# Kernel optimization log

Hardware: AMD Instinct MI355X
Metric: run time of the kernel (lower is better)

Reference implementation:

```python
import jax, jax.numpy as jnp
import numpy as np


def setup_inputs() -> dict:
    key = jax.random.key(0)
    k1, k2, k3 = jax.random.split(key, 3)
    x = jax.random.normal(k1, (32, 256, 56, 56), dtype=jnp.float32)
    att_w = jax.random.normal(k2, (4, 256), dtype=jnp.float32) * 0.05  # 1x1 attention conv weight (K, Cin)
    weight = jax.random.normal(k3, (4, 256, 256, 3, 3), dtype=jnp.float32) * 0.05  # (K, Cout, Cin, kh, kw)
    return {"x": x, "att_w": att_w, "weight": weight}


def reference(x, att_w, weight):
    # x: (B, Cin, H, W); att_w: (K, Cin); weight: (K, Cout, Cin, kh, kw)
    # Attention: global avg pool -> 1x1 conv (Cin->K) -> sigmoid  (named softmax_att but is sigmoid)
    pooled = jnp.mean(x, axis=(2, 3))                 # (B, Cin)
    att = jax.nn.sigmoid(pooled @ att_w.T)            # (B, K)
    # Per-sample expert-mixed conv kernels
    agg_w = jnp.einsum('bk,koihw->boihw', att, weight)  # (B, Cout, Cin, kh, kw)

    def conv_one(xi, wi):
        # xi: (Cin, H, W), wi: (Cout, Cin, kh, kw)
        return jax.lax.conv_general_dilated(
            xi[None], wi,
            window_strides=(1, 1),
            padding=[(1, 1), (1, 1)],
            rhs_dilation=(1, 1),
            dimension_numbers=('NCHW', 'OIHW', 'NCHW'),
        )[0]

    out = jax.vmap(conv_one)(x, agg_w)                # (B, Cout, H, W)
    return out
```

## Files before the change

kernel.cpp:

```cpp
#include <hip/hip_runtime.h>

typedef __attribute__((ext_vector_type(8))) short short8;
typedef __attribute__((ext_vector_type(4))) float floatx4;

__device__ __forceinline__ unsigned short bf16_rne(float f) {
  unsigned int u = __builtin_bit_cast(unsigned int, f);
  u += 0x7fffu + ((u >> 16) & 1u);
  return (unsigned short)(u >> 16);
}

__device__ __forceinline__ void glds16(const void* g, void* l) {
  __builtin_amdgcn_global_load_lds((const __attribute__((address_space(1))) void*)g,
                                   (__attribute__((address_space(3))) void*)l, 16, 0, 0);
}


__global__ void zero_pk_kernel(float* __restrict__ pk) {
  pk[threadIdx.x] = 0.f;
}

__global__ __launch_bounds__(256) void prep_kernel(const float* __restrict__ x,
                                                   const float* __restrict__ att_w,
                                                   unsigned short* __restrict__ xpad,
                                                   float* __restrict__ pooledk) {
  const int bid = blockIdx.x;
  const int b   = bid / 196;
  const int rem = bid - b * 196;
  const int cig = rem / 49;
  const int spc = rem - cig * 49;
  const int t  = threadIdx.x;
  const int cs = t >> 6, sl = t & 63;
  const int sp0 = spc * 64;

  __shared__ unsigned short T2[64 * 72];
  __shared__ float red[4][4];

  const float* xrow = x + (size_t)(b * 256 + cig * 64 + cs * 16) * 3136 + sp0 + sl;
  float v[16];
  #pragma unroll
  for (int i = 0; i < 16; ++i) v[i] = xrow[(size_t)i * 3136];

  float acc0 = 0.f, acc1 = 0.f, acc2 = 0.f, acc3 = 0.f;
  #pragma unroll
  for (int i = 0; i < 16; ++i) {
    const int ci = cig * 64 + cs * 16 + i;
    acc0 += v[i] * att_w[0 * 256 + ci];
    acc1 += v[i] * att_w[1 * 256 + ci];
    acc2 += v[i] * att_w[2 * 256 + ci];
    acc3 += v[i] * att_w[3 * 256 + ci];
  }
  #pragma unroll
  for (int o = 32; o > 0; o >>= 1) {
    acc0 += __shfl_xor(acc0, o, 64);
    acc1 += __shfl_xor(acc1, o, 64);
    acc2 += __shfl_xor(acc2, o, 64);
    acc3 += __shfl_xor(acc3, o, 64);
  }
  if (sl == 0) { red[cs][0] = acc0; red[cs][1] = acc1; red[cs][2] = acc2; red[cs][3] = acc3; }

  short8 w0, w1;
  #pragma unroll
  for (int i = 0; i < 8; ++i) w0[i] = (short)bf16_rne(v[i]);
  #pragma unroll
  for (int i = 0; i < 8; ++i) w1[i] = (short)bf16_rne(v[8 + i]);
  *(short8*)(T2 + sl * 72 + cs * 16) = w0;
  *(short8*)(T2 + sl * 72 + cs * 16 + 8) = w1;
  __syncthreads();

  if (t < 4) {
    float s = red[0][t] + red[1][t] + red[2][t] + red[3][t];
    atomicAdd(&pooledk[b * 4 + t], s);
  }

  unsigned short* xb = xpad + (size_t)b * (8 * 3364 * 32);
  #pragma unroll
  for (int it = 0; it < 2; ++it) {
    const int c = it * 256 + t;
    const int spl = c >> 3, oc8 = c & 7;
    const int cg8 = cig * 8 + oc8;
    const int kc = cg8 >> 2, o2 = cg8 & 3;
    const int spg = sp0 + spl;
    const int h = spg / 56, wc = spg - h * 56;
    const int pos = (h + 1) * 58 + (wc + 1);
    const short8 vv = *(const short8*)(T2 + spl * 72 + oc8 * 8);
    *(short8*)(xb + (size_t)kc * (3364 * 32) + pos * 32 + o2 * 8) = vv;
  }
}

__global__ __launch_bounds__(256) void border_kernel(unsigned short* __restrict__ xpad) {
  const int b = blockIdx.x, quarter = blockIdx.y, t = threadIdx.x;
  const short8 z = {0, 0, 0, 0, 0, 0, 0, 0};
  unsigned short* xb = xpad + (size_t)b * (8 * 3364 * 32);
  for (int it = 0; it < 8; ++it) {
    const int idx = it * 256 + t;
    if (idx >= 1824) break;
    const int s8 = idx & 3, kc = (idx >> 2) & 7, j = idx >> 5;
    const int pi = quarter * 57 + j;
    int h2, w2;
    if (pi < 58)       { h2 = 0;  w2 = pi; }
    else if (pi < 116) { h2 = 57; w2 = pi - 58; }
    else { const int k = pi - 116; h2 = 1 + (k >> 1); w2 = (k & 1) * 57; }
    *(short8*)(xb + (size_t)kc * (3364 * 32) + (h2 * 58 + w2) * 32 + s8 * 8) = z;
  }
}

__global__ __launch_bounds__(256) void agg_kernel(const float* __restrict__ w,
                                                  const float* __restrict__ pooledk,
                                                  unsigned short* __restrict__ agg) {
  const int co = blockIdx.x;
  const int bq = blockIdx.y;
  const int t = threadIdx.x;
  __shared__ float W[4][2304];
  __shared__ float attl[16];
  if (t < 16) {
    const float z = pooledk[bq * 16 + t] * (1.f / 3136.f);
    attl[t] = 1.f / (1.f + expf(-z));
  }
  #pragma unroll
  for (int e = 0; e < 4; ++e) {
    const float* src = w + (size_t)(e * 256 + co) * 2304;
    #pragma unroll
    for (int j = 0; j < 9; ++j) W[e][j * 256 + t] = src[j * 256 + t];
  }
  __syncthreads();

  #pragma unroll
  for (int rep = 0; rep < 2; ++rep) {
    const int id = rep * 256 + t;
    if (id < 288) {
      const int kc  = id / 36;
      const int rm  = id - kc * 36;
      const int rs  = rm >> 2;
      const int oct = rm & 3;
      const int wib = (kc * 32 + oct * 8) * 9 + rs;
      const int off = (kc * 9 + rs) * 8192 + co * 32 + oct * 8;
      float w0[8], w1[8], w2[8], w3[8];
      #pragma unroll
      for (int u = 0; u < 8; ++u) {
        w0[u] = W[0][wib + u * 9];
        w1[u] = W[1][wib + u * 9];
        w2[u] = W[2][wib + u * 9];
        w3[u] = W[3][wib + u * 9];
      }
      #pragma unroll
      for (int bl = 0; bl < 4; ++bl) {
        const int b = bq * 4 + bl;
        const float a0 = attl[bl * 4 + 0], a1 = attl[bl * 4 + 1];
        const float a2 = attl[bl * 4 + 2], a3 = attl[bl * 4 + 3];
        short8 vv;
        #pragma unroll
        for (int u = 0; u < 8; ++u)
          vv[u] = (short)bf16_rne(a0 * w0[u] + a1 * w1[u] + a2 * w2[u] + a3 * w3[u]);
        *(short8*)(agg + (size_t)b * 589824 + off) = vv;
      }
    }
  }
}

__global__ __launch_bounds__(256) void conv_kernel(const unsigned short* __restrict__ xpad,
                                                   const unsigned short* __restrict__ aggw,
                                                   float* __restrict__ out) {
  __shared__ unsigned short Bsm[348 * 32];
  __shared__ unsigned short Asm[3 * 128 * 32];

  const int t  = threadIdx.x;
  const int bx0 = blockIdx.x;
  const int bx  = (bx0 & 7) * 200 + (bx0 >> 3);
  const int p_t  = bx % 25;
  const int co_t = (bx / 25) & 1;
  const int b    = bx / 50;
  const int p0   = p_t * 128;
  const int oh_min = p0 / 56;

  const unsigned short* xb  = xpad + (size_t)b * (8 * 3364 * 32);
  const unsigned short* awb = aggw + (size_t)b * 589824 + co_t * 4096;

  const int lane = t & 63;
  const int wv = t >> 6;
  const int wm = wv >> 1;
  const int wn = wv & 1;
  const int m16 = lane & 15;
  const int q = lane >> 4;

  int aoff[4], boff[4];
  #pragma unroll
  for (int i = 0; i < 4; ++i)
    aoff[i] = (wm * 64 + i * 16 + m16) * 32 + q * 8;
  #pragma unroll
  for (int j = 0; j < 4; ++j) {
    const int pf = p0 + wn * 64 + j * 16 + m16;
    const int oh = pf / 56;
    const int ow = pf - oh * 56;
    boff[j] = ((oh - oh_min) * 58 + ow) * 32 + q * 8;
  }

  floatx4 acc[4][4];
  #pragma unroll
  for (int i = 0; i < 4; ++i)
    #pragma unroll
    for (int j = 0; j < 4; ++j)
      acc[i][j] = (floatx4){0.f, 0.f, 0.f, 0.f};

  for (int kc = 0; kc < 8; ++kc) {
    const unsigned short* xkc = xb + (size_t)kc * (3364 * 32);
    #pragma unroll
    for (int i = 0; i < 6; ++i) {
      const int c = i * 256 + t;
      if (c < 1392) {
        const int pos = c >> 2, sub = c & 3;
        const int prow = pos / 58;
        const int pcol = pos - prow * 58;
        int ih2 = oh_min + prow; if (ih2 > 57) ih2 = 57;
        glds16(xkc + ((size_t)(ih2 * 58 + pcol) * 32 + sub * 8), (void*)(Bsm + c * 8));
      }
    }
    #pragma unroll
    for (int g = 0; g < 3; ++g) {
      #pragma unroll
      for (int i = 0; i < 6; ++i) {
        const int c = i * 256 + t;
        const int rsl = c >> 9;
        const int w5 = c & 511;
        glds16(awb + (size_t)(kc * 9 + g * 3 + rsl) * 8192 + w5 * 8, (void*)(Asm + c * 8));
      }
      __syncthreads();

      #pragma unroll
      for (int rsl = 0; rsl < 3; ++rsl) {
        const int d = (g * 58 + rsl) * 32;
        short8 af[4], bf[4];
        #pragma unroll
        for (int i = 0; i < 4; ++i)
          af[i] = *(const short8*)(Asm + rsl * 4096 + aoff[i]);
        #pragma unroll
        for (int j = 0; j < 4; ++j)
          bf[j] = *(const short8*)(Bsm + boff[j] + d);
        #pragma unroll
        for (int i = 0; i < 4; ++i)
          #pragma unroll
          for (int j = 0; j < 4; ++j)
            acc[i][j] = __builtin_amdgcn_mfma_f32_16x16x32_bf16(af[i], bf[j], acc[i][j], 0, 0, 0);
      }
      __syncthreads();
    }
  }

  #pragma unroll
  for (int i = 0; i < 4; ++i) {
    const int co = co_t * 128 + wm * 64 + i * 16 + q * 4;
    float* orow = out + (size_t)(b * 256 + co) * 3136;
    #pragma unroll
    for (int j = 0; j < 4; ++j) {
      const int pp = p0 + wn * 64 + j * 16 + m16;
      if (pp < 3136) {
        #pragma unroll
        for (int rg = 0; rg < 4; ++rg)
          orow[(size_t)rg * 3136 + pp] = acc[i][j][rg];
      }
    }
  }
}

extern "C" void kernel_launch(void* const* d_in, const int* in_sizes, int n_in,
                              void* d_out, int out_size, void* d_ws, size_t ws_size,
                              hipStream_t stream) {
  const float* x      = (const float*)d_in[0];
  const float* att_w  = (const float*)d_in[1];
  const float* weight = (const float*)d_in[2];
  float* out = (float*)d_out;

  char* ws = (char*)d_ws;
  float* pooledk       = (float*)ws;
  unsigned short* agg  = (unsigned short*)(ws + 65536);
  unsigned short* xpad = (unsigned short*)(ws + 65536 + 37748736);

  zero_pk_kernel<<<1, 128, 0, stream>>>(pooledk);
  prep_kernel<<<6272, 256, 0, stream>>>(x, att_w, xpad, pooledk);
  border_kernel<<<dim3(32, 4), 256, 0, stream>>>(xpad);
  agg_kernel<<<dim3(256, 8), 256, 0, stream>>>(weight, pooledk, agg);
  conv_kernel<<<1600, 256, 0, stream>>>(xpad, agg, out);
}
```

Baseline: 308.8 us.

## Double-buffer weight tiles, XOR-swizzle LDS, and fold border zeroing into prep

The conv kernel now double-buffers the A (aggregated weight) LDS tile, prefetching the next slice while MFMAs run on the current one. It uses manual vmcnt waits, raw barriers and setprio in place of __syncthreads. Both A and B LDS tiles get an XOR swizzle on the 16-byte chunk index to reduce bank conflicts on fragment reads. The separate border-zeroing launch is folded into a subset of prep_kernel blocks, which removes one kernel launch. This uses more LDS and relies on hand-counted vmcnt values, which are fragile.

```diff
diff --git a/kernel.cpp b/kernel.cpp
--- a/kernel.cpp
+++ b/kernel.cpp
@@ -85,22 +85,21 @@
     const short8 vv = *(const short8*)(T2 + spl * 72 + oc8 * 8);
     *(short8*)(xb + (size_t)kc * (3364 * 32) + pos * 32 + o2 * 8) = vv;
   }
-}
-
-__global__ __launch_bounds__(256) void border_kernel(unsigned short* __restrict__ xpad) {
-  const int b = blockIdx.x, quarter = blockIdx.y, t = threadIdx.x;
-  const short8 z = {0, 0, 0, 0, 0, 0, 0, 0};
-  unsigned short* xb = xpad + (size_t)b * (8 * 3364 * 32);
-  for (int it = 0; it < 8; ++it) {
-    const int idx = it * 256 + t;
-    if (idx >= 1824) break;
-    const int s8 = idx & 3, kc = (idx >> 2) & 7, j = idx >> 5;
-    const int pi = quarter * 57 + j;
-    int h2, w2;
-    if (pi < 58)       { h2 = 0;  w2 = pi; }
-    else if (pi < 116) { h2 = 57; w2 = pi - 58; }
-    else { const int k = pi - 116; h2 = 1 + (k >> 1); w2 = (k & 1) * 57; }
-    *(short8*)(xb + (size_t)kc * (3364 * 32) + (h2 * 58 + w2) * 32 + s8 * 8) = z;
+
+  if (cig == 0 && spc < 4) {
+    const short8 z = {0, 0, 0, 0, 0, 0, 0, 0};
+    #pragma unroll
+    for (int it = 0; it < 8; ++it) {
+      const int idx = it * 256 + t;
+      if (idx >= 1824) break;
+      const int s8 = idx & 3, kc = (idx >> 2) & 7, j = idx >> 5;
+      const int pi = spc * 57 + j;
+      int h2, w2;
+      if (pi < 58)       { h2 = 0;  w2 = pi; }
+      else if (pi < 116) { h2 = 57; w2 = pi - 58; }
+      else { const int k = pi - 116; h2 = 1 + (k >> 1); w2 = (k & 1) * 57; }
+      *(short8*)(xb + (size_t)kc * (3364 * 32) + (h2 * 58 + w2) * 32 + s8 * 8) = z;
+    }
   }
 }
 
@@ -157,11 +156,40 @@
   }
 }
 
+__device__ __forceinline__ void stageA(const unsigned short* __restrict__ awb,
+                                       unsigned short* As, int slice_base, int t) {
+  #pragma unroll
+  for (int i = 0; i < 6; ++i) {
+    const int c = i * 256 + t;
+    const int rsl = c >> 9;
+    const int w5 = c & 511;
+    const int row = w5 >> 2, qc = w5 & 3;
+    const int qg = qc ^ (row & 3) ^ ((row >> 2) & 3);
+    glds16(awb + (size_t)(slice_base + rsl) * 8192 + (row * 4 + qg) * 8, (void*)(As + c * 8));
+  }
+}
+
+__device__ __forceinline__ void stageB(const unsigned short* __restrict__ xkc,
+                                       unsigned short* Bs, int oh_min, int t) {
+  #pragma unroll
+  for (int i = 0; i < 6; ++i) {
+    const int c = i * 256 + t;
+    if (c < 1392) {
+      const int pos = c >> 2, sub = c & 3;
+      const int subg = sub ^ (pos & 3) ^ ((pos >> 2) & 3);
+      const int prow = pos / 58;
+      const int pcol = pos - prow * 58;
+      int ih2 = oh_min + prow; if (ih2 > 57) ih2 = 57;
+      glds16(xkc + ((size_t)(ih2 * 58 + pcol) * 32 + subg * 8), (void*)(Bs + c * 8));
+    }
+  }
+}
+
 __global__ __launch_bounds__(256) void conv_kernel(const unsigned short* __restrict__ xpad,
                                                    const unsigned short* __restrict__ aggw,
                                                    float* __restrict__ out) {
-  __shared__ unsigned short Bsm[348 * 32];
-  __shared__ unsigned short Asm[3 * 128 * 32];
+  __shared__ alignas(16) unsigned short Bsm[348 * 32];
+  __shared__ alignas(16) unsigned short Asm[2][3 * 128 * 32];
 
   const int t  = threadIdx.x;
   const int bx0 = blockIdx.x;
@@ -182,16 +210,19 @@
   const int m16 = lane & 15;
   const int q = lane >> 4;
 
-  int aoff[4], boff[4];
-  #pragma unroll
-  for (int i = 0; i < 4; ++i)
-    aoff[i] = (wm * 64 + i * 16 + m16) * 32 + q * 8;
+  int aoff[4], brow[4];
+  #pragma unroll
+  for (int i = 0; i < 4; ++i) {
+    const int row = wm * 64 + i * 16 + m16;
+    const int qg = q ^ (row & 3) ^ ((row >> 2) & 3);
+    aoff[i] = row * 32 + qg * 8;
+  }
   #pragma unroll
   for (int j = 0; j < 4; ++j) {
     const int pf = p0 + wn * 64 + j * 16 + m16;
     const int oh = pf / 56;
     const int ow = pf - oh * 56;
-    boff[j] = ((oh - oh_min) * 58 + ow) * 32 + q * 8;
+    brow[j] = (oh - oh_min) * 58 + ow;
   }
 
   floatx4 acc[4][4];
@@ -201,47 +232,52 @@
     for (int j = 0; j < 4; ++j)
       acc[i][j] = (floatx4){0.f, 0.f, 0.f, 0.f};
 
+  stageB(xb, Bsm, oh_min, t);
+  stageA(awb, Asm[0], 0, t);
+
   for (int kc = 0; kc < 8; ++kc) {
-    const unsigned short* xkc = xb + (size_t)kc * (3364 * 32);
-    #pragma unroll
-    for (int i = 0; i < 6; ++i) {
-      const int c = i * 256 + t;
-      if (c < 1392) {
-        const int pos = c >> 2, sub = c & 3;
-        const int prow = pos / 58;
-        const int pcol = pos - prow * 58;
-        int ih2 = oh_min + prow; if (ih2 > 57) ih2 = 57;
-        glds16(xkc + ((size_t)(ih2 * 58 + pcol) * 32 + sub * 8), (void*)(Bsm + c * 8));
-      }
-    }
     #pragma unroll
     for (int g = 0; g < 3; ++g) {
-      #pragma unroll
-      for (int i = 0; i < 6; ++i) {
-        const int c = i * 256 + t;
-        const int rsl = c >> 9;
-        const int w5 = c & 511;
-        glds16(awb + (size_t)(kc * 9 + g * 3 + rsl) * 8192 + w5 * 8, (void*)(Asm + c * 8));
-      }
-      __syncthreads();
-
+      const int gi = kc * 3 + g;
+      unsigned short* Acur = Asm[gi & 1];
+      unsigned short* Anxt = Asm[(gi + 1) & 1];
+      if (g < 2) {
+        stageA(awb, Anxt, kc * 9 + (g + 1) * 3, t);
+        asm volatile("s_waitcnt vmcnt(6)" ::: "memory");
+      } else {
+        asm volatile("s_waitcnt vmcnt(0)" ::: "memory");
+      }
+      __builtin_amdgcn_s_barrier();
+      __builtin_amdgcn_sched_barrier(0);
+
+      __builtin_amdgcn_s_setprio(1);
       #pragma unroll
       for (int rsl = 0; rsl < 3; ++rsl) {
-        const int d = (g * 58 + rsl) * 32;
-        short8 af[4], bf[4];
+        const int shift = g * 58 + rsl;
+        short8 af[4], bfr[4];
         #pragma unroll
         for (int i = 0; i < 4; ++i)
-          af[i] = *(const short8*)(Asm + rsl * 4096 + aoff[i]);
-        #pragma unroll
-        for (int j = 0; j < 4; ++j)
-          bf[j] = *(const short8*)(Bsm + boff[j] + d);
+          af[i] = *(const short8*)(Acur + rsl * 4096 + aoff[i]);
+        #pragma unroll
+        for (int j = 0; j < 4; ++j) {
+          const int row = brow[j] + shift;
+          const int bq = q ^ (row & 3) ^ ((row >> 2) & 3);
+          bfr[j] = *(const short8*)(Bsm + row * 32 + bq * 8);
+        }
         #pragma unroll
         for (int i = 0; i < 4; ++i)
           #pragma unroll
           for (int j = 0; j < 4; ++j)
-            acc[i][j] = __builtin_amdgcn_mfma_f32_16x16x32_bf16(af[i], bf[j], acc[i][j], 0, 0, 0);
-      }
-      __syncthreads();
+            acc[i][j] = __builtin_amdgcn_mfma_f32_16x16x32_bf16(af[i], bfr[j], acc[i][j], 0, 0, 0);
+      }
+      __builtin_amdgcn_s_setprio(0);
+
+      __builtin_amdgcn_sched_barrier(0);
+      __builtin_amdgcn_s_barrier();
+      if (g == 2 && kc < 7) {
+        stageB(xb + (size_t)(kc + 1) * (3364 * 32), Bsm, oh_min, t);
+        stageA(awb, Anxt, (kc + 1) * 9, t);
+      }
     }
   }
 
@@ -276,7 +312,6 @@
 
   zero_pk_kernel<<<1, 128, 0, stream>>>(pooledk);
   prep_kernel<<<6272, 256, 0, stream>>>(x, att_w, xpad, pooledk);
-  border_kernel<<<dim3(32, 4), 256, 0, stream>>>(xpad);
   agg_kernel<<<dim3(256, 8), 256, 0, stream>>>(weight, pooledk, agg);
   conv_kernel<<<1600, 256, 0, stream>>>(xpad, agg, out);
 }
```

Measured after the change: 379.6 us. 22.9% more time.

## Double-buffer input tile in conv, read weights directly, fold border zeroing into prep

Applied to the files above, without the earlier changes.

The conv kernel now double-buffers the padded-input tile in LDS, prefetching the next channel chunk while computing the current one, with one barrier per chunk instead of two per filter row. Weight fragments are loaded straight from global memory rather than staged through LDS. Border zeroing moves into the prep kernel, removing a launch, and prep's store pattern is reordered for more contiguous writes. The trade-off is uncoalesced, uncached-in-LDS weight reads and a hint targeting three blocks per SIMD, which could limit registers.

```diff
diff --git a/kernel.cpp b/kernel.cpp
--- a/kernel.cpp
+++ b/kernel.cpp
@@ -75,32 +75,30 @@
   unsigned short* xb = xpad + (size_t)b * (8 * 3364 * 32);
   #pragma unroll
   for (int it = 0; it < 2; ++it) {
-    const int c = it * 256 + t;
-    const int spl = c >> 3, oc8 = c & 7;
-    const int cg8 = cig * 8 + oc8;
-    const int kc = cg8 >> 2, o2 = cg8 & 3;
+    const int c9 = it * 256 + t;
+    const int o2 = c9 & 3, spl = (c9 >> 2) & 63, kcsel = c9 >> 8;
+    const int kc = cig * 2 + kcsel;
     const int spg = sp0 + spl;
     const int h = spg / 56, wc = spg - h * 56;
     const int pos = (h + 1) * 58 + (wc + 1);
-    const short8 vv = *(const short8*)(T2 + spl * 72 + oc8 * 8);
+    const short8 vv = *(const short8*)(T2 + spl * 72 + (kcsel * 4 + o2) * 8);
     *(short8*)(xb + (size_t)kc * (3364 * 32) + pos * 32 + o2 * 8) = vv;
   }
-}
-
-__global__ __launch_bounds__(256) void border_kernel(unsigned short* __restrict__ xpad) {
-  const int b = blockIdx.x, quarter = blockIdx.y, t = threadIdx.x;
-  const short8 z = {0, 0, 0, 0, 0, 0, 0, 0};
-  unsigned short* xb = xpad + (size_t)b * (8 * 3364 * 32);
-  for (int it = 0; it < 8; ++it) {
-    const int idx = it * 256 + t;
-    if (idx >= 1824) break;
-    const int s8 = idx & 3, kc = (idx >> 2) & 7, j = idx >> 5;
-    const int pi = quarter * 57 + j;
-    int h2, w2;
-    if (pi < 58)       { h2 = 0;  w2 = pi; }
-    else if (pi < 116) { h2 = 57; w2 = pi - 58; }
-    else { const int k = pi - 116; h2 = 1 + (k >> 1); w2 = (k & 1) * 57; }
-    *(short8*)(xb + (size_t)kc * (3364 * 32) + (h2 * 58 + w2) * 32 + s8 * 8) = z;
+
+  if (cig == 0 && spc < 4) {
+    const short8 z = {0, 0, 0, 0, 0, 0, 0, 0};
+    #pragma unroll
+    for (int it = 0; it < 8; ++it) {
+      const int idx = it * 256 + t;
+      if (idx >= 1824) break;
+      const int s8 = idx & 3, kc = (idx >> 2) & 7, j = idx >> 5;
+      const int pi = spc * 57 + j;
+      int h2, w2;
+      if (pi < 58)       { h2 = 0;  w2 = pi; }
+      else if (pi < 116) { h2 = 57; w2 = pi - 58; }
+      else { const int k = pi - 116; h2 = 1 + (k >> 1); w2 = (k & 1) * 57; }
+      *(short8*)(xb + (size_t)kc * (3364 * 32) + (h2 * 58 + w2) * 32 + s8 * 8) = z;
+    }
   }
 }
 
@@ -157,11 +155,25 @@
   }
 }
 
-__global__ __launch_bounds__(256) void conv_kernel(const unsigned short* __restrict__ xpad,
-                                                   const unsigned short* __restrict__ aggw,
-                                                   float* __restrict__ out) {
-  __shared__ unsigned short Bsm[348 * 32];
-  __shared__ unsigned short Asm[3 * 128 * 32];
+__device__ __forceinline__ void stageB(const unsigned short* __restrict__ xkc,
+                                       unsigned short* Bs, int oh_min, int t) {
+  #pragma unroll
+  for (int i = 0; i < 6; ++i) {
+    const int c = i * 256 + t;
+    if (c < 1392) {
+      const int pos = c >> 2, sub = c & 3;
+      const int prow = pos / 58;
+      const int pcol = pos - prow * 58;
+      int ih2 = oh_min + prow; if (ih2 > 57) ih2 = 57;
+      glds16(xkc + ((size_t)(ih2 * 58 + pcol) * 32 + sub * 8), (void*)(Bs + c * 8));
+    }
+  }
+}
+
+__global__ __launch_bounds__(256, 3) void conv_kernel(const unsigned short* __restrict__ xpad,
+                                                      const unsigned short* __restrict__ aggw,
+                                                      float* __restrict__ out) {
+  __shared__ alignas(16) unsigned short Bsm[2][348 * 32];
 
   const int t  = threadIdx.x;
   const int bx0 = blockIdx.x;
@@ -182,7 +194,7 @@
   const int m16 = lane & 15;
   const int q = lane >> 4;
 
-  int aoff[4], boff[4];
+  int aoff[4], brow[4];
   #pragma unroll
   for (int i = 0; i < 4; ++i)
     aoff[i] = (wm * 64 + i * 16 + m16) * 32 + q * 8;
@@ -191,7 +203,7 @@
     const int pf = p0 + wn * 64 + j * 16 + m16;
     const int oh = pf / 56;
     const int ow = pf - oh * 56;
-    boff[j] = ((oh - oh_min) * 58 + ow) * 32 + q * 8;
+    brow[j] = ((oh - oh_min) * 58 + ow) * 32 + q * 8;
   }
 
   floatx4 acc[4][4];
@@ -201,48 +213,33 @@
     for (int j = 0; j < 4; ++j)
       acc[i][j] = (floatx4){0.f, 0.f, 0.f, 0.f};
 
+  stageB(xb, Bsm[0], oh_min, t);
+  __syncthreads();
+
   for (int kc = 0; kc < 8; ++kc) {
-    const unsigned short* xkc = xb + (size_t)kc * (3364 * 32);
-    #pragma unroll
-    for (int i = 0; i < 6; ++i) {
-      const int c = i * 256 + t;
-      if (c < 1392) {
-        const int pos = c >> 2, sub = c & 3;
-        const int prow = pos / 58;
-        const int pcol = pos - prow * 58;
-        int ih2 = oh_min + prow; if (ih2 > 57) ih2 = 57;
-        glds16(xkc + ((size_t)(ih2 * 58 + pcol) * 32 + sub * 8), (void*)(Bsm + c * 8));
-      }
-    }
-    #pragma unroll
-    for (int g = 0; g < 3; ++g) {
-      #pragma unroll
-      for (int i = 0; i < 6; ++i) {
-        const int c = i * 256 + t;
-        const int rsl = c >> 9;
-        const int w5 = c & 511;
-        glds16(awb + (size_t)(kc * 9 + g * 3 + rsl) * 8192 + w5 * 8, (void*)(Asm + c * 8));
-      }
-      __syncthreads();
-
-      #pragma unroll
-      for (int rsl = 0; rsl < 3; ++rsl) {
-        const int d = (g * 58 + rsl) * 32;
-        short8 af[4], bf[4];
-        #pragma unroll
-        for (int i = 0; i < 4; ++i)
-          af[i] = *(const short8*)(Asm + rsl * 4096 + aoff[i]);
+    const unsigned short* Bcur = Bsm[kc & 1];
+    if (kc < 7)
+      stageB(xb + (size_t)(kc + 1) * (3364 * 32), Bsm[(kc + 1) & 1], oh_min, t);
+
+    const unsigned short* aslab = awb + (size_t)kc * 9 * 8192;
+    #pragma unroll
+    for (int rs = 0; rs < 9; ++rs) {
+      const int r = rs / 3, s = rs - r * 3;
+      const int d = (r * 58 + s) * 32;
+      short8 af[4], bfr[4];
+      #pragma unroll
+      for (int i = 0; i < 4; ++i)
+        af[i] = *(const short8*)(aslab + (size_t)rs * 8192 + aoff[i]);
+      #pragma unroll
+      for (int j = 0; j < 4; ++j)
+        bfr[j] = *(const short8*)(Bcur + brow[j] + d);
+      #pragma unroll
+      for (int i = 0; i < 4; ++i)
         #pragma unroll
         for (int j = 0; j < 4; ++j)
-          bf[j] = *(const short8*)(Bsm + boff[j] + d);
-        #pragma unroll
-        for (int i = 0; i < 4; ++i)
-          #pragma unroll
-          for (int j = 0; j < 4; ++j)
-            acc[i][j] = __builtin_amdgcn_mfma_f32_16x16x32_bf16(af[i], bf[j], acc[i][j], 0, 0, 0);
-      }
-      __syncthreads();
-    }
+          acc[i][j] = __builtin_amdgcn_mfma_f32_16x16x32_bf16(af[i], bfr[j], acc[i][j], 0, 0, 0);
+    }
+    __syncthreads();
   }
 
   #pragma unroll
@@ -276,7 +273,6 @@
 
   zero_pk_kernel<<<1, 128, 0, stream>>>(pooledk);
   prep_kernel<<<6272, 256, 0, stream>>>(x, att_w, xpad, pooledk);
-  border_kernel<<<dim3(32, 4), 256, 0, stream>>>(xpad);
   agg_kernel<<<dim3(256, 8), 256, 0, stream>>>(weight, pooledk, agg);
   conv_kernel<<<1600, 256, 0, stream>>>(xpad, agg, out);
 }
```

Measured after the change: 366.5 us. 18.7% more time.

## Vectorize prep loads, pad atomic counters, fold border zeroing into prep kernel

Applied to the files above, without the earlier changes.

The prep kernel now loads x as float4 vectors, so each thread covers 4 channels by 4 spatial positions instead of 16 channels by 1 position, and the pooled sum is formed from pre-summed vectors. The transpose into shared memory and the write-out are re-indexed to match. Pooled accumulators are spread 16 floats apart so atomics from different batch/expert pairs land in separate cache lines. Border zeroing moves into a subset of prep blocks, which removes one kernel launch. The cost is a less regular LDS write pattern (4-short stores), and a few blocks now do extra border work.

```diff
diff --git a/kernel.cpp b/kernel.cpp
--- a/kernel.cpp
+++ b/kernel.cpp
@@ -2,6 +2,7 @@
 
 typedef __attribute__((ext_vector_type(8))) short short8;
 typedef __attribute__((ext_vector_type(4))) float floatx4;
+typedef __attribute__((ext_vector_type(4))) unsigned short ush4;
 
 __device__ __forceinline__ unsigned short bf16_rne(float f) {
   unsigned int u = __builtin_bit_cast(unsigned int, f);
@@ -16,7 +17,8 @@
 
 
 __global__ void zero_pk_kernel(float* __restrict__ pk) {
-  pk[threadIdx.x] = 0.f;
+  #pragma unroll
+  for (int i = 0; i < 8; ++i) pk[i * 256 + threadIdx.x] = 0.f;
 }
 
 __global__ __launch_bounds__(256) void prep_kernel(const float* __restrict__ x,
@@ -35,19 +37,22 @@
   __shared__ unsigned short T2[64 * 72];
   __shared__ float red[4][4];
 
-  const float* xrow = x + (size_t)(b * 256 + cig * 64 + cs * 16) * 3136 + sp0 + sl;
-  float v[16];
-  #pragma unroll
-  for (int i = 0; i < 16; ++i) v[i] = xrow[(size_t)i * 3136];
+  const int qd = sl >> 4;
+  const int sx = sl & 15;
+  const float* xrow = x + (size_t)(b * 256 + cig * 64 + cs * 16 + qd * 4) * 3136 + sp0 + sx * 4;
+  floatx4 v4[4];
+  #pragma unroll
+  for (int i = 0; i < 4; ++i) v4[i] = *(const floatx4*)(xrow + (size_t)i * 3136);
 
   float acc0 = 0.f, acc1 = 0.f, acc2 = 0.f, acc3 = 0.f;
   #pragma unroll
-  for (int i = 0; i < 16; ++i) {
-    const int ci = cig * 64 + cs * 16 + i;
-    acc0 += v[i] * att_w[0 * 256 + ci];
-    acc1 += v[i] * att_w[1 * 256 + ci];
-    acc2 += v[i] * att_w[2 * 256 + ci];
-    acc3 += v[i] * att_w[3 * 256 + ci];
+  for (int i = 0; i < 4; ++i) {
+    const float sv = v4[i][0] + v4[i][1] + v4[i][2] + v4[i][3];
+    const float* aw = att_w + (cig * 64 + cs * 16 + qd * 4 + i);
+    acc0 += sv * aw[0];
+    acc1 += sv * aw[256];
+    acc2 += sv * aw[512];
+    acc3 += sv * aw[768];
   }
   #pragma unroll
   for (int o = 32; o > 0; o >>= 1) {
@@ -58,49 +63,49 @@
   }
   if (sl == 0) { red[cs][0] = acc0; red[cs][1] = acc1; red[cs][2] = acc2; red[cs][3] = acc3; }
 
-  short8 w0, w1;
-  #pragma unroll
-  for (int i = 0; i < 8; ++i) w0[i] = (short)bf16_rne(v[i]);
-  #pragma unroll
-  for (int i = 0; i < 8; ++i) w1[i] = (short)bf16_rne(v[8 + i]);
-  *(short8*)(T2 + sl * 72 + cs * 16) = w0;
-  *(short8*)(T2 + sl * 72 + cs * 16 + 8) = w1;
+  #pragma unroll
+  for (int s = 0; s < 4; ++s) {
+    ush4 wv;
+    wv[0] = bf16_rne(v4[0][s]);
+    wv[1] = bf16_rne(v4[1][s]);
+    wv[2] = bf16_rne(v4[2][s]);
+    wv[3] = bf16_rne(v4[3][s]);
+    *(ush4*)(T2 + (sx * 4 + s) * 72 + cs * 16 + qd * 4) = wv;
+  }
   __syncthreads();
 
   if (t < 4) {
     float s = red[0][t] + red[1][t] + red[2][t] + red[3][t];
-    atomicAdd(&pooledk[b * 4 + t], s);
+    atomicAdd(&pooledk[(b * 4 + t) * 16], s);
   }
 
   unsigned short* xb = xpad + (size_t)b * (8 * 3364 * 32);
   #pragma unroll
   for (int it = 0; it < 2; ++it) {
-    const int c = it * 256 + t;
-    const int spl = c >> 3, oc8 = c & 7;
-    const int cg8 = cig * 8 + oc8;
-    const int kc = cg8 >> 2, o2 = cg8 & 3;
+    const int c9 = it * 256 + t;
+    const int o2 = c9 & 3, spl = (c9 >> 2) & 63, kcsel = c9 >> 8;
+    const int kc = cig * 2 + kcsel;
     const int spg = sp0 + spl;
     const int h = spg / 56, wc = spg - h * 56;
     const int pos = (h + 1) * 58 + (wc + 1);
-    const short8 vv = *(const short8*)(T2 + spl * 72 + oc8 * 8);
+    const short8 vv = *(const short8*)(T2 + spl * 72 + (kcsel * 4 + o2) * 8);
     *(short8*)(xb + (size_t)kc * (3364 * 32) + pos * 32 + o2 * 8) = vv;
   }
-}
-
-__global__ __launch_bounds__(256) void border_kernel(unsigned short* __restrict__ xpad) {
-  const int b = blockIdx.x, quarter = blockIdx.y, t = threadIdx.x;
-  const short8 z = {0, 0, 0, 0, 0, 0, 0, 0};
-  unsigned short* xb = xpad + (size_t)b * (8 * 3364 * 32);
-  for (int it = 0; it < 8; ++it) {
-    const int idx = it * 256 + t;
-    if (idx >= 1824) break;
-    const int s8 = idx & 3, kc = (idx >> 2) & 7, j = idx >> 5;
-    const int pi = quarter * 57 + j;
-    int h2, w2;
-    if (pi < 58)       { h2 = 0;  w2 = pi; }
-    else if (pi < 116) { h2 = 57; w2 = pi - 58; }
-    else { const int k = pi - 116; h2 = 1 + (k >> 1); w2 = (k & 1) * 57; }
-    *(short8*)(xb + (size_t)kc * (3364 * 32) + (h2 * 58 + w2) * 32 + s8 * 8) = z;
+
+  if (cig == 0 && spc < 4) {
+    const short8 z = {0, 0, 0, 0, 0, 0, 0, 0};
+    #pragma unroll
+    for (int it = 0; it < 8; ++it) {
+      const int idx = it * 256 + t;
+      if (idx >= 1824) break;
+      const int s8 = idx & 3, kc = (idx >> 2) & 7, j = idx >> 5;
+      const int pi = spc * 57 + j;
+      int h2, w2;
+      if (pi < 58)       { h2 = 0;  w2 = pi; }
+      else if (pi < 116) { h2 = 57; w2 = pi - 58; }
+      else { const int k = pi - 116; h2 = 1 + (k >> 1); w2 = (k & 1) * 57; }
+      *(short8*)(xb + (size_t)kc * (3364 * 32) + (h2 * 58 + w2) * 32 + s8 * 8) = z;
+    }
   }
 }
 
@@ -113,7 +118,7 @@
   __shared__ float W[4][2304];
   __shared__ float attl[16];
   if (t < 16) {
-    const float z = pooledk[bq * 16 + t] * (1.f / 3136.f);
+    const float z = pooledk[(bq * 16 + t) * 16] * (1.f / 3136.f);
     attl[t] = 1.f / (1.f + expf(-z));
   }
   #pragma unroll
@@ -274,9 +279,8 @@
   unsigned short* agg  = (unsigned short*)(ws + 65536);
   unsigned short* xpad = (unsigned short*)(ws + 65536 + 37748736);
 
-  zero_pk_kernel<<<1, 128, 0, stream>>>(pooledk);
+  zero_pk_kernel<<<1, 256, 0, stream>>>(pooledk);
   prep_kernel<<<6272, 256, 0, stream>>>(x, att_w, xpad, pooledk);
-  border_kernel<<<dim3(32, 4), 256, 0, stream>>>(xpad);
   agg_kernel<<<dim3(256, 8), 256, 0, stream>>>(weight, pooledk, agg);
   conv_kernel<<<1600, 256, 0, stream>>>(xpad, agg, out);
 }
```

Result: faster. 302.4 us (-2.1%).
